# Optimization experiments

Hardware: AMD Instinct MI355X
Metric: run time of the kernel (lower is better)

## Reference

```python
import jax, jax.numpy as jnp
import numpy as np

B, S, D_IN, D_OUT, R = 8, 2048, 2048, 2048, 16

def setup_inputs() -> dict:
    key = jax.random.key(0)
    k = jax.random.split(key, 5)
    scale_w = 1.0 / np.sqrt(D_IN)
    return {
        "x": jax.random.normal(k[0], (B, S, D_IN), dtype=jnp.float32),
        "A_params": jax.random.normal(k[1], (B, D_OUT, R), dtype=jnp.float32) * 0.02,
        "B_params": jax.random.normal(k[2], (B, R, D_IN), dtype=jnp.float32) * 0.02,
        "W": jax.random.normal(k[3], (D_OUT, D_IN), dtype=jnp.float32) * scale_w,
        "b": jax.random.normal(k[4], (D_OUT,), dtype=jnp.float32) * scale_w,
    }

def reference(x, A_params, B_params, W, b):
    # base: x @ W^T + b  -> [B, S, out]
    base_out = jnp.einsum("bsi,oi->bso", x, W) + b
    # intermediate = x @ B^T -> [B, S, r]
    intermediate = jnp.einsum("bsi,bri->bsr", x, B_params)
    # adaptation = intermediate @ A^T -> [B, S, out]
    adaptation = jnp.einsum("bsr,bor->bso", intermediate, A_params)
    return base_out + adaptation
```

## Files before the change

kernel.cpp:

```cpp
#include <hip/hip_runtime.h>
#include <cstdint>
#include <cstddef>

typedef __attribute__((ext_vector_type(4))) float  floatx4;
typedef __attribute__((ext_vector_type(8))) __bf16 bf16x8;
typedef __attribute__((ext_vector_type(8))) unsigned short u16x8;

#define M_TOT 16384
#define N_TOT 2048
#define K_TOT 2048
#define NBATCH 8
#define RLORA 16

__device__ __forceinline__ unsigned short f32_to_bf16(float f) {
  unsigned u = __float_as_uint(f);
  u += 0x7fffu + ((u >> 16) & 1u);
  return (unsigned short)(u >> 16);
}

#define GLOAD_LDS16(gp, lp)                                                        \
  __builtin_amdgcn_global_load_lds((__attribute__((address_space(1))) void*)(void*)(gp), \
                                   (__attribute__((address_space(3))) void*)(void*)(lp), \
                                   16, 0, 0)

__global__ void k_convert(const float* __restrict__ in, unsigned short* __restrict__ out, int n8) {
  int i = blockIdx.x * blockDim.x + threadIdx.x;
  if (i >= n8) return;
  const float4* p = (const float4*)in + (size_t)i * 2;
  float4 v0 = p[0], v1 = p[1];
  u16x8 o;
  o[0] = f32_to_bf16(v0.x); o[1] = f32_to_bf16(v0.y);
  o[2] = f32_to_bf16(v0.z); o[3] = f32_to_bf16(v0.w);
  o[4] = f32_to_bf16(v1.x); o[5] = f32_to_bf16(v1.y);
  o[6] = f32_to_bf16(v1.z); o[7] = f32_to_bf16(v1.w);
  *(u16x8*)(out + (size_t)i * 8) = o;
}

__global__ void k_convert_a(const float* __restrict__ A, unsigned short* __restrict__ abf) {
  int row = blockIdx.x * blockDim.x + threadIdx.x;
  if (row >= NBATCH * N_TOT) return;
  const float4* p = (const float4*)(A + (size_t)row * RLORA);
  float4 v0 = p[0], v1 = p[1], v2 = p[2], v3 = p[3];
  u16x8 lo, hi2, z = {0,0,0,0,0,0,0,0};
  lo[0] = f32_to_bf16(v0.x); lo[1] = f32_to_bf16(v0.y);
  lo[2] = f32_to_bf16(v0.z); lo[3] = f32_to_bf16(v0.w);
  lo[4] = f32_to_bf16(v1.x); lo[5] = f32_to_bf16(v1.y);
  lo[6] = f32_to_bf16(v1.z); lo[7] = f32_to_bf16(v1.w);
  hi2[0] = f32_to_bf16(v2.x); hi2[1] = f32_to_bf16(v2.y);
  hi2[2] = f32_to_bf16(v2.z); hi2[3] = f32_to_bf16(v2.w);
  hi2[4] = f32_to_bf16(v3.x); hi2[5] = f32_to_bf16(v3.y);
  hi2[6] = f32_to_bf16(v3.z); hi2[7] = f32_to_bf16(v3.w);
  u16x8* dst = (u16x8*)(abf + (size_t)row * 32);
  dst[0] = lo; dst[1] = hi2; dst[2] = z; dst[3] = z;
}

__global__ __launch_bounds__(256) void k_inter(const unsigned short* __restrict__ xbf,
                                               const unsigned short* __restrict__ bpbf,
                                               unsigned short* __restrict__ interbf) {
  const int tid  = threadIdx.x;
  const int lane = tid & 63;
  const int wv   = tid >> 6;
  const int l15  = lane & 15;
  const int hi   = lane >> 4;
  const int m0   = blockIdx.x * 64;
  const int bb   = m0 >> 11;

  floatx4 zero = {0.f, 0.f, 0.f, 0.f};
  floatx4 acc[4] = {zero, zero, zero, zero};

  const unsigned short* bpb = bpbf + (size_t)bb * (RLORA * K_TOT);
  const int kb0 = wv * 512;
  for (int kb = kb0; kb < kb0 + 512; kb += 32) {
    bf16x8 bfr = *(const bf16x8*)(bpb + (size_t)l15 * K_TOT + kb + hi * 8);
    #pragma unroll
    for (int mi = 0; mi < 4; ++mi) {
      bf16x8 afr = *(const bf16x8*)(xbf + (size_t)(m0 + mi * 16 + l15) * K_TOT + kb + hi * 8);
      acc[mi] = __builtin_amdgcn_mfma_f32_16x16x32_bf16(afr, bfr, acc[mi], 0, 0, 0);
    }
  }

  __shared__ floatx4 red[4][4][64];
  #pragma unroll
  for (int mi = 0; mi < 4; ++mi) red[wv][mi][lane] = acc[mi];
  __syncthreads();
  if (wv == 0) {
    #pragma unroll
    for (int mi = 0; mi < 4; ++mi) {
      floatx4 s = red[0][mi][lane] + red[1][mi][lane] + red[2][mi][lane] + red[3][mi][lane];
      #pragma unroll
      for (int j = 0; j < 4; ++j) {
        int m = m0 + mi * 16 + hi * 4 + j;
        interbf[(size_t)m * 32 + l15] = f32_to_bf16(s[j]);
        interbf[(size_t)m * 32 + 16 + l15] = 0;
      }
    }
  }
}

__global__ __launch_bounds__(256) void k_gemm(const unsigned short* __restrict__ xbf,
                                              const unsigned short* __restrict__ wbf,
                                              const unsigned short* __restrict__ interbf,
                                              const unsigned short* __restrict__ abf,
                                              const float* __restrict__ bias,
                                              float* __restrict__ out) {
  __shared__ unsigned short As[128 * 64];
  __shared__ unsigned short Bs[128 * 64];
  const int tid  = threadIdx.x;
  const int lane = tid & 63;
  const int wv   = tid >> 6;
  const int wm   = wv >> 1, wn = wv & 1;
  const int l15  = lane & 15;
  const int hi   = lane >> 4;

  int bid  = blockIdx.x;
  int swzb = ((bid & 7) << 8) | (bid >> 3);
  const int mt = swzb >> 4;
  const int nt = swzb & 15;
  const int mrow0 = mt << 7;
  const int ncol0 = nt << 7;
  const int bb = mrow0 >> 11;

  const int m0 = mrow0 + wm * 64;
  const int n0 = ncol0 + wn * 64;

  floatx4 acc[4][4];
  {
    bf16x8 la[4], lb[4];
    #pragma unroll
    for (int mi = 0; mi < 4; ++mi)
      la[mi] = *(const bf16x8*)(interbf + (size_t)(m0 + mi * 16 + l15) * 32 + hi * 8);
    #pragma unroll
    for (int ni = 0; ni < 4; ++ni)
      lb[ni] = *(const bf16x8*)(abf + ((size_t)bb * N_TOT + n0 + ni * 16 + l15) * 32 + hi * 8);
    floatx4 z = {0.f, 0.f, 0.f, 0.f};
    #pragma unroll
    for (int mi = 0; mi < 4; ++mi)
      #pragma unroll
      for (int ni = 0; ni < 4; ++ni)
        acc[mi][ni] = __builtin_amdgcn_mfma_f32_16x16x32_bf16(la[mi], lb[ni], z, 0, 0, 0);
  }

  const unsigned short* Ag = xbf + (size_t)mrow0 * K_TOT;
  const unsigned short* Bg = wbf + (size_t)ncol0 * K_TOT;
  const unsigned short* pA[4];
  const unsigned short* pB[4];
  int ldsOff[4];
  #pragma unroll
  for (int i = 0; i < 4; ++i) {
    int c   = i * 256 + wv * 64 + lane;
    int row = c >> 3;
    int k8  = (c & 7) ^ (row & 7);
    pA[i] = Ag + (size_t)row * K_TOT + k8 * 8;
    pB[i] = Bg + (size_t)row * K_TOT + k8 * 8;
    ldsOff[i] = (i * 256 + wv * 64) * 16;
  }

  for (int kt = 0; kt < K_TOT; kt += 64) {
    #pragma unroll
    for (int i = 0; i < 4; ++i) GLOAD_LDS16(pA[i] + kt, (char*)As + ldsOff[i]);
    #pragma unroll
    for (int i = 0; i < 4; ++i) GLOAD_LDS16(pB[i] + kt, (char*)Bs + ldsOff[i]);
    asm volatile("s_waitcnt vmcnt(0)" ::: "memory");
    __syncthreads();

    #pragma unroll
    for (int ks = 0; ks < 2; ++ks) {
      bf16x8 af[4], bfv[4];
      #pragma unroll
      for (int mi = 0; mi < 4; ++mi) {
        int row = wm * 64 + mi * 16 + l15;
        int k8  = (ks * 4 + hi) ^ (row & 7);
        af[mi] = *(const bf16x8*)((const char*)As + row * 128 + k8 * 16);
      }
      #pragma unroll
      for (int ni = 0; ni < 4; ++ni) {
        int row = wn * 64 + ni * 16 + l15;
        int k8  = (ks * 4 + hi) ^ (row & 7);
        bfv[ni] = *(const bf16x8*)((const char*)Bs + row * 128 + k8 * 16);
      }
      #pragma unroll
      for (int mi = 0; mi < 4; ++mi)
        #pragma unroll
        for (int ni = 0; ni < 4; ++ni)
          acc[mi][ni] = __builtin_amdgcn_mfma_f32_16x16x32_bf16(af[mi], bfv[ni], acc[mi][ni], 0, 0, 0);
    }
    __syncthreads();
  }

  #pragma unroll
  for (int ni = 0; ni < 4; ++ni) {
    int col = n0 + ni * 16 + l15;
    float bv = bias[col];
    #pragma unroll
    for (int mi = 0; mi < 4; ++mi) {
      int r0 = m0 + mi * 16 + hi * 4;
      #pragma unroll
      for (int j = 0; j < 4; ++j)
        out[(size_t)(r0 + j) * N_TOT + col] = acc[mi][ni][j] + bv;
    }
  }
}

extern "C" void kernel_launch(void* const* d_in, const int* in_sizes, int n_in,
                              void* d_out, int out_size, void* d_ws, size_t ws_size,
                              hipStream_t stream) {
  const float* x    = (const float*)d_in[0];
  const float* Ap   = (const float*)d_in[1];
  const float* Bp   = (const float*)d_in[2];
  const float* W    = (const float*)d_in[3];
  const float* bias = (const float*)d_in[4];
  float* out = (float*)d_out;

  char* ws = (char*)d_ws;
  unsigned short* xbf     = (unsigned short*)(ws);
  unsigned short* wbf     = (unsigned short*)(ws + 67108864);
  unsigned short* abf     = (unsigned short*)(ws + 67108864 + 8388608);
  unsigned short* bpbf    = (unsigned short*)(ws + 67108864 + 8388608 + 1048576);
  unsigned short* interbf = (unsigned short*)(ws + 67108864 + 8388608 + 1048576 + 524288);

  k_convert<<<dim3(16384), dim3(256), 0, stream>>>(x,  xbf,  4194304);
  k_convert<<<dim3(2048),  dim3(256), 0, stream>>>(W,  wbf,   524288);
  k_convert<<<dim3(128),   dim3(256), 0, stream>>>(Bp, bpbf,   32768);
  k_convert_a<<<dim3(64),  dim3(256), 0, stream>>>(Ap, abf);

  k_inter<<<dim3(256), dim3(256), 0, stream>>>(xbf, bpbf, interbf);

  k_gemm<<<dim3(2048), dim3(256), 0, stream>>>(xbf, wbf, interbf, abf, bias, out);
}
```

Measured before the change: 200.5 us.

## Rewrite main GEMM as 256x256 tile, 8-wave, double-buffered pipelined kernel

Tiles grow from 128x128 with 4 waves to 256x256 with 8 waves. Each wave now computes a 128x64 sub-tile. Global-to-LDS loads are double-buffered and staged in quarter-tile pieces interleaved with four MFMA phases, using barriers, partial vmcnt waits and s_setprio to overlap memory with compute. This replaces the old load-wait-compute loop that exposed latency every k-step, and raises arithmetic intensity per LDS byte. The cost is more registers (32 accumulators per wave), 64KB of LDS per block, and intricate hand-scheduled synchronization that may hide hazards.

```diff
diff --git a/kernel.cpp b/kernel.cpp
--- a/kernel.cpp
+++ b/kernel.cpp
@@ -11,6 +11,7 @@
 #define K_TOT 2048
 #define NBATCH 8
 #define RLORA 16
+#define NT 32
 
 __device__ __forceinline__ unsigned short f32_to_bf16(float f) {
   unsigned u = __float_as_uint(f);
@@ -22,6 +23,8 @@
   __builtin_amdgcn_global_load_lds((__attribute__((address_space(1))) void*)(void*)(gp), \
                                    (__attribute__((address_space(3))) void*)(void*)(lp), \
                                    16, 0, 0)
+
+template<int V> struct IC { static constexpr int value = V; };
 
 __global__ void k_convert(const float* __restrict__ in, unsigned short* __restrict__ out, int n8) {
   int i = blockIdx.x * blockDim.x + threadIdx.x;
@@ -97,106 +100,169 @@
   }
 }
 
-__global__ __launch_bounds__(256) void k_gemm(const unsigned short* __restrict__ xbf,
-                                              const unsigned short* __restrict__ wbf,
-                                              const unsigned short* __restrict__ interbf,
-                                              const unsigned short* __restrict__ abf,
-                                              const float* __restrict__ bias,
-                                              float* __restrict__ out) {
-  __shared__ unsigned short As[128 * 64];
-  __shared__ unsigned short Bs[128 * 64];
+#define STAGE_A(bufi, h, tt) do {                                                      \
+  GLOAD_LDS16(Ag + (h)*262144 + (tt)*64 + gOff0, AsB + ((bufi)*2+(h))*16384 + ldsB0);  \
+  GLOAD_LDS16(Ag + (h)*262144 + (tt)*64 + gOff1, AsB + ((bufi)*2+(h))*16384 + ldsB1);  \
+} while(0)
+#define STAGE_B(bufi, h, tt) do {                                                      \
+  GLOAD_LDS16(Bg + (h)*262144 + (tt)*64 + gOff0, BsB + ((bufi)*2+(h))*16384 + ldsB0);  \
+  GLOAD_LDS16(Bg + (h)*262144 + (tt)*64 + gOff1, BsB + ((bufi)*2+(h))*16384 + ldsB1);  \
+} while(0)
+#define LDA(bufi, qm, mi, ks) (*(const bf16x8*)(AsB + ((bufi)*2 + wm)*16384 + \
+  ((qm)*64 + (mi)*16 + l15)*128 + ((((ks)*4 + hi) ^ swz) * 16)))
+#define LDB(bufi, ni, ks)     (*(const bf16x8*)(BsB + ((bufi)*2 + (wn>>1))*16384 + \
+  (((wn&1)*64 + (ni)*16 + l15)*128 + ((((ks)*4 + hi) ^ swz) * 16))))
+
+__global__ __launch_bounds__(512, 2) void k_gemm(const unsigned short* __restrict__ xbf,
+                                                 const unsigned short* __restrict__ wbf,
+                                                 const unsigned short* __restrict__ interbf,
+                                                 const unsigned short* __restrict__ abf,
+                                                 const float* __restrict__ bias,
+                                                 float* __restrict__ out) {
+  __shared__ unsigned short As[2][2][8192];
+  __shared__ unsigned short Bs[2][2][8192];
   const int tid  = threadIdx.x;
   const int lane = tid & 63;
-  const int wv   = tid >> 6;
-  const int wm   = wv >> 1, wn = wv & 1;
+  const int wid  = tid >> 6;
+  const int wm   = wid >> 2;
+  const int wn   = wid & 3;
   const int l15  = lane & 15;
   const int hi   = lane >> 4;
+  const int swz  = l15 & 7;
 
   int bid  = blockIdx.x;
-  int swzb = ((bid & 7) << 8) | (bid >> 3);
-  const int mt = swzb >> 4;
-  const int nt = swzb & 15;
-  const int mrow0 = mt << 7;
-  const int ncol0 = nt << 7;
+  int swzb = ((bid & 7) << 6) | (bid >> 3);
+  const int mt = swzb >> 3;
+  const int nt = swzb & 7;
+  const int mrow0 = mt << 8;
+  const int ncol0 = nt << 8;
   const int bb = mrow0 >> 11;
 
-  const int m0 = mrow0 + wm * 64;
+  const int m0 = mrow0 + wm * 128;
   const int n0 = ncol0 + wn * 64;
 
-  floatx4 acc[4][4];
+  const unsigned short* Ag = xbf + (size_t)mrow0 * K_TOT;
+  const unsigned short* Bg = wbf + (size_t)ncol0 * K_TOT;
+  char* AsB = (char*)As;
+  char* BsB = (char*)Bs;
+
+  const int r0    = tid >> 3;
+  const int k80   = (tid & 7) ^ (r0 & 7);
+  const int gOff0 = r0 * K_TOT + k80 * 8;
+  const int gOff1 = gOff0 + 64 * K_TOT;
+  const int ldsB0 = wid * 1024;
+  const int ldsB1 = 8192 + wid * 1024;
+
+  floatx4 acc[8][4];
   {
-    bf16x8 la[4], lb[4];
-    #pragma unroll
-    for (int mi = 0; mi < 4; ++mi)
+    bf16x8 la[8], lb[4];
+    #pragma unroll
+    for (int mi = 0; mi < 8; ++mi)
       la[mi] = *(const bf16x8*)(interbf + (size_t)(m0 + mi * 16 + l15) * 32 + hi * 8);
     #pragma unroll
     for (int ni = 0; ni < 4; ++ni)
       lb[ni] = *(const bf16x8*)(abf + ((size_t)bb * N_TOT + n0 + ni * 16 + l15) * 32 + hi * 8);
+
+    STAGE_B(0, 0, 0); STAGE_B(0, 1, 0); STAGE_A(0, 0, 0); STAGE_A(0, 1, 0);
+    STAGE_B(1, 0, 1); STAGE_B(1, 1, 1); STAGE_A(1, 0, 1);
+
     floatx4 z = {0.f, 0.f, 0.f, 0.f};
     #pragma unroll
-    for (int mi = 0; mi < 4; ++mi)
+    for (int mi = 0; mi < 8; ++mi)
       #pragma unroll
       for (int ni = 0; ni < 4; ++ni)
         acc[mi][ni] = __builtin_amdgcn_mfma_f32_16x16x32_bf16(la[mi], lb[ni], z, 0, 0, 0);
   }
-
-  const unsigned short* Ag = xbf + (size_t)mrow0 * K_TOT;
-  const unsigned short* Bg = wbf + (size_t)ncol0 * K_TOT;
-  const unsigned short* pA[4];
-  const unsigned short* pB[4];
-  int ldsOff[4];
-  #pragma unroll
-  for (int i = 0; i < 4; ++i) {
-    int c   = i * 256 + wv * 64 + lane;
-    int row = c >> 3;
-    int k8  = (c & 7) ^ (row & 7);
-    pA[i] = Ag + (size_t)row * K_TOT + k8 * 8;
-    pB[i] = Bg + (size_t)row * K_TOT + k8 * 8;
-    ldsOff[i] = (i * 256 + wv * 64) * 16;
-  }
-
-  for (int kt = 0; kt < K_TOT; kt += 64) {
-    #pragma unroll
-    for (int i = 0; i < 4; ++i) GLOAD_LDS16(pA[i] + kt, (char*)As + ldsOff[i]);
-    #pragma unroll
-    for (int i = 0; i < 4; ++i) GLOAD_LDS16(pB[i] + kt, (char*)Bs + ldsOff[i]);
-    asm volatile("s_waitcnt vmcnt(0)" ::: "memory");
-    __syncthreads();
-
-    #pragma unroll
-    for (int ks = 0; ks < 2; ++ks) {
-      bf16x8 af[4], bfv[4];
-      #pragma unroll
-      for (int mi = 0; mi < 4; ++mi) {
-        int row = wm * 64 + mi * 16 + l15;
-        int k8  = (ks * 4 + hi) ^ (row & 7);
-        af[mi] = *(const bf16x8*)((const char*)As + row * 128 + k8 * 16);
-      }
-      #pragma unroll
-      for (int ni = 0; ni < 4; ++ni) {
-        int row = wn * 64 + ni * 16 + l15;
-        int k8  = (ks * 4 + hi) ^ (row & 7);
-        bfv[ni] = *(const bf16x8*)((const char*)Bs + row * 128 + k8 * 16);
-      }
-      #pragma unroll
-      for (int mi = 0; mi < 4; ++mi)
-        #pragma unroll
-        for (int ni = 0; ni < 4; ++ni)
-          acc[mi][ni] = __builtin_amdgcn_mfma_f32_16x16x32_bf16(af[mi], bfv[ni], acc[mi][ni], 0, 0, 0);
-    }
-    __syncthreads();
-  }
+  asm volatile("s_waitcnt vmcnt(6)" ::: "memory");
+  __builtin_amdgcn_s_barrier();
+
+  auto tile = [&](int t, auto s1_, auto s2_, auto vm_) {
+    constexpr int S1 = decltype(s1_)::value;
+    constexpr int S2 = decltype(s2_)::value;
+    constexpr int VM = decltype(vm_)::value;
+    const int buf = t & 1;
+    bf16x8 af[4][2], bfr[4][2];
+
+    #pragma unroll
+    for (int mi = 0; mi < 4; ++mi) { af[mi][0] = LDA(buf, 0, mi, 0); af[mi][1] = LDA(buf, 0, mi, 1); }
+    #pragma unroll
+    for (int ni = 0; ni < 2; ++ni) { bfr[ni][0] = LDB(buf, ni, 0); bfr[ni][1] = LDB(buf, ni, 1); }
+    if constexpr (S1) STAGE_A(buf ^ 1, 1, t + 1);
+    __builtin_amdgcn_s_barrier();
+    asm volatile("s_waitcnt lgkmcnt(0)" ::: "memory");
+    __builtin_amdgcn_s_setprio(1);
+    #pragma unroll
+    for (int mi = 0; mi < 4; ++mi)
+      #pragma unroll
+      for (int ni = 0; ni < 2; ++ni) {
+        acc[mi][ni] = __builtin_amdgcn_mfma_f32_16x16x32_bf16(af[mi][0], bfr[ni][0], acc[mi][ni], 0, 0, 0);
+        acc[mi][ni] = __builtin_amdgcn_mfma_f32_16x16x32_bf16(af[mi][1], bfr[ni][1], acc[mi][ni], 0, 0, 0);
+      }
+    __builtin_amdgcn_s_setprio(0);
+    __builtin_amdgcn_s_barrier();
+
+    #pragma unroll
+    for (int ni = 0; ni < 2; ++ni) { bfr[2+ni][0] = LDB(buf, 2+ni, 0); bfr[2+ni][1] = LDB(buf, 2+ni, 1); }
+    __builtin_amdgcn_s_barrier();
+    asm volatile("s_waitcnt lgkmcnt(0)" ::: "memory");
+    __builtin_amdgcn_s_setprio(1);
+    #pragma unroll
+    for (int mi = 0; mi < 4; ++mi)
+      #pragma unroll
+      for (int ni = 0; ni < 2; ++ni) {
+        acc[mi][2+ni] = __builtin_amdgcn_mfma_f32_16x16x32_bf16(af[mi][0], bfr[2+ni][0], acc[mi][2+ni], 0, 0, 0);
+        acc[mi][2+ni] = __builtin_amdgcn_mfma_f32_16x16x32_bf16(af[mi][1], bfr[2+ni][1], acc[mi][2+ni], 0, 0, 0);
+      }
+    __builtin_amdgcn_s_setprio(0);
+    __builtin_amdgcn_s_barrier();
+
+    #pragma unroll
+    for (int mi = 0; mi < 4; ++mi) { af[mi][0] = LDA(buf, 1, mi, 0); af[mi][1] = LDA(buf, 1, mi, 1); }
+    if constexpr (S2) { STAGE_B(buf, 0, t + 2); STAGE_B(buf, 1, t + 2); }
+    __builtin_amdgcn_s_barrier();
+    asm volatile("s_waitcnt lgkmcnt(0)" ::: "memory");
+    __builtin_amdgcn_s_setprio(1);
+    #pragma unroll
+    for (int mi = 0; mi < 4; ++mi)
+      #pragma unroll
+      for (int ni = 0; ni < 2; ++ni) {
+        acc[4+mi][ni] = __builtin_amdgcn_mfma_f32_16x16x32_bf16(af[mi][0], bfr[ni][0], acc[4+mi][ni], 0, 0, 0);
+        acc[4+mi][ni] = __builtin_amdgcn_mfma_f32_16x16x32_bf16(af[mi][1], bfr[ni][1], acc[4+mi][ni], 0, 0, 0);
+      }
+    __builtin_amdgcn_s_setprio(0);
+    __builtin_amdgcn_s_barrier();
+
+    if constexpr (S2) STAGE_A(buf, 0, t + 2);
+    __builtin_amdgcn_s_barrier();
+    asm volatile("s_waitcnt lgkmcnt(0)" ::: "memory");
+    __builtin_amdgcn_s_setprio(1);
+    #pragma unroll
+    for (int mi = 0; mi < 4; ++mi)
+      #pragma unroll
+      for (int ni = 0; ni < 2; ++ni) {
+        acc[4+mi][2+ni] = __builtin_amdgcn_mfma_f32_16x16x32_bf16(af[mi][0], bfr[2+ni][0], acc[4+mi][2+ni], 0, 0, 0);
+        acc[4+mi][2+ni] = __builtin_amdgcn_mfma_f32_16x16x32_bf16(af[mi][1], bfr[2+ni][1], acc[4+mi][2+ni], 0, 0, 0);
+      }
+    __builtin_amdgcn_s_setprio(0);
+    if constexpr (VM == 6)      asm volatile("s_waitcnt vmcnt(6)" ::: "memory");
+    else if constexpr (VM == 0) asm volatile("s_waitcnt vmcnt(0)" ::: "memory");
+    __builtin_amdgcn_s_barrier();
+  };
+
+  for (int t = 0; t < NT - 2; ++t) tile(t, IC<1>{}, IC<1>{}, IC<6>{});
+  tile(NT - 2, IC<1>{}, IC<0>{}, IC<0>{});
+  tile(NT - 1, IC<0>{}, IC<0>{}, IC<-1>{});
 
   #pragma unroll
   for (int ni = 0; ni < 4; ++ni) {
     int col = n0 + ni * 16 + l15;
     float bv = bias[col];
     #pragma unroll
-    for (int mi = 0; mi < 4; ++mi) {
-      int r0 = m0 + mi * 16 + hi * 4;
+    for (int mi = 0; mi < 8; ++mi) {
+      int r = m0 + mi * 16 + hi * 4;
       #pragma unroll
       for (int j = 0; j < 4; ++j)
-        out[(size_t)(r0 + j) * N_TOT + col] = acc[mi][ni][j] + bv;
+        out[(size_t)(r + j) * N_TOT + col] = acc[mi][ni][j] + bv;
     }
   }
 }
@@ -225,5 +291,5 @@
 
   k_inter<<<dim3(256), dim3(256), 0, stream>>>(xbf, bpbf, interbf);
 
-  k_gemm<<<dim3(2048), dim3(256), 0, stream>>>(xbf, wbf, interbf, abf, bias, out);
-}
+  k_gemm<<<dim3(512), dim3(512), 0, stream>>>(xbf, wbf, interbf, abf, bias, out);
+}
```

Measured after the change: 210.0 us. +4.7%, slower.

## Fuse LoRA intermediate projection into main GEMM and merge conversion kernels

Applied to the files above, without the earlier changes.

Removes the separate k_inter kernel. The x@B^T LoRA projection is now computed inside the main GEMM k-loop, reusing the x tiles already staged in LDS, and the B_params slice is streamed into a small extra LDS buffer. The intermediate is written to LDS and applied with A after the loop instead of as an initial MFMA. The W/B/A conversions are also merged into one launch, and the x conversion loops over 8 elements per thread. This saves a full extra read of bf16 x and two launches, at the cost of redundant intermediate MFMAs across the 16 N-tiles and extra LDS traffic per iteration.

```diff
diff --git a/kernel.cpp b/kernel.cpp
--- a/kernel.cpp
+++ b/kernel.cpp
@@ -18,99 +18,68 @@
   return (unsigned short)(u >> 16);
 }
 
+__device__ __forceinline__ u16x8 cvt8(const float4& a, const float4& b) {
+  u16x8 o;
+  o[0] = f32_to_bf16(a.x); o[1] = f32_to_bf16(a.y);
+  o[2] = f32_to_bf16(a.z); o[3] = f32_to_bf16(a.w);
+  o[4] = f32_to_bf16(b.x); o[5] = f32_to_bf16(b.y);
+  o[6] = f32_to_bf16(b.z); o[7] = f32_to_bf16(b.w);
+  return o;
+}
+
 #define GLOAD_LDS16(gp, lp)                                                        \
   __builtin_amdgcn_global_load_lds((__attribute__((address_space(1))) void*)(void*)(gp), \
                                    (__attribute__((address_space(3))) void*)(void*)(lp), \
                                    16, 0, 0)
 
-__global__ void k_convert(const float* __restrict__ in, unsigned short* __restrict__ out, int n8) {
-  int i = blockIdx.x * blockDim.x + threadIdx.x;
-  if (i >= n8) return;
-  const float4* p = (const float4*)in + (size_t)i * 2;
-  float4 v0 = p[0], v1 = p[1];
-  u16x8 o;
-  o[0] = f32_to_bf16(v0.x); o[1] = f32_to_bf16(v0.y);
-  o[2] = f32_to_bf16(v0.z); o[3] = f32_to_bf16(v0.w);
-  o[4] = f32_to_bf16(v1.x); o[5] = f32_to_bf16(v1.y);
-  o[6] = f32_to_bf16(v1.z); o[7] = f32_to_bf16(v1.w);
-  *(u16x8*)(out + (size_t)i * 8) = o;
-}
-
-__global__ void k_convert_a(const float* __restrict__ A, unsigned short* __restrict__ abf) {
-  int row = blockIdx.x * blockDim.x + threadIdx.x;
-  if (row >= NBATCH * N_TOT) return;
-  const float4* p = (const float4*)(A + (size_t)row * RLORA);
-  float4 v0 = p[0], v1 = p[1], v2 = p[2], v3 = p[3];
-  u16x8 lo, hi2, z = {0,0,0,0,0,0,0,0};
-  lo[0] = f32_to_bf16(v0.x); lo[1] = f32_to_bf16(v0.y);
-  lo[2] = f32_to_bf16(v0.z); lo[3] = f32_to_bf16(v0.w);
-  lo[4] = f32_to_bf16(v1.x); lo[5] = f32_to_bf16(v1.y);
-  lo[6] = f32_to_bf16(v1.z); lo[7] = f32_to_bf16(v1.w);
-  hi2[0] = f32_to_bf16(v2.x); hi2[1] = f32_to_bf16(v2.y);
-  hi2[2] = f32_to_bf16(v2.z); hi2[3] = f32_to_bf16(v2.w);
-  hi2[4] = f32_to_bf16(v3.x); hi2[5] = f32_to_bf16(v3.y);
-  hi2[6] = f32_to_bf16(v3.z); hi2[7] = f32_to_bf16(v3.w);
-  u16x8* dst = (u16x8*)(abf + (size_t)row * 32);
-  dst[0] = lo; dst[1] = hi2; dst[2] = z; dst[3] = z;
-}
-
-__global__ __launch_bounds__(256) void k_inter(const unsigned short* __restrict__ xbf,
-                                               const unsigned short* __restrict__ bpbf,
-                                               unsigned short* __restrict__ interbf) {
-  const int tid  = threadIdx.x;
-  const int lane = tid & 63;
-  const int wv   = tid >> 6;
-  const int l15  = lane & 15;
-  const int hi   = lane >> 4;
-  const int m0   = blockIdx.x * 64;
-  const int bb   = m0 >> 11;
-
-  floatx4 zero = {0.f, 0.f, 0.f, 0.f};
-  floatx4 acc[4] = {zero, zero, zero, zero};
-
-  const unsigned short* bpb = bpbf + (size_t)bb * (RLORA * K_TOT);
-  const int kb0 = wv * 512;
-  for (int kb = kb0; kb < kb0 + 512; kb += 32) {
-    bf16x8 bfr = *(const bf16x8*)(bpb + (size_t)l15 * K_TOT + kb + hi * 8);
-    #pragma unroll
-    for (int mi = 0; mi < 4; ++mi) {
-      bf16x8 afr = *(const bf16x8*)(xbf + (size_t)(m0 + mi * 16 + l15) * K_TOT + kb + hi * 8);
-      acc[mi] = __builtin_amdgcn_mfma_f32_16x16x32_bf16(afr, bfr, acc[mi], 0, 0, 0);
-    }
-  }
-
-  __shared__ floatx4 red[4][4][64];
-  #pragma unroll
-  for (int mi = 0; mi < 4; ++mi) red[wv][mi][lane] = acc[mi];
-  __syncthreads();
-  if (wv == 0) {
-    #pragma unroll
-    for (int mi = 0; mi < 4; ++mi) {
-      floatx4 s = red[0][mi][lane] + red[1][mi][lane] + red[2][mi][lane] + red[3][mi][lane];
-      #pragma unroll
-      for (int j = 0; j < 4; ++j) {
-        int m = m0 + mi * 16 + hi * 4 + j;
-        interbf[(size_t)m * 32 + l15] = f32_to_bf16(s[j]);
-        interbf[(size_t)m * 32 + 16 + l15] = 0;
-      }
-    }
+__global__ void k_convert_x(const float* __restrict__ in, unsigned short* __restrict__ out) {
+  int i0 = blockIdx.x * blockDim.x + threadIdx.x;
+  #pragma unroll
+  for (int it = 0; it < 8; ++it) {
+    size_t i = (size_t)i0 + (size_t)it * 524288;
+    const float4* p = (const float4*)in + i * 2;
+    *(u16x8*)(out + i * 8) = cvt8(p[0], p[1]);
+  }
+}
+
+__global__ void k_convert_small(const float* __restrict__ W, const float* __restrict__ Bp,
+                                const float* __restrict__ Ap,
+                                unsigned short* __restrict__ wbf, unsigned short* __restrict__ bpbf,
+                                unsigned short* __restrict__ abf) {
+  int b = blockIdx.x;
+  if (b < 2048) {
+    int i = b * 256 + threadIdx.x;
+    const float4* p = (const float4*)W + (size_t)i * 2;
+    *(u16x8*)(wbf + (size_t)i * 8) = cvt8(p[0], p[1]);
+  } else if (b < 2176) {
+    int i = (b - 2048) * 256 + threadIdx.x;
+    const float4* p = (const float4*)Bp + (size_t)i * 2;
+    *(u16x8*)(bpbf + (size_t)i * 8) = cvt8(p[0], p[1]);
+  } else {
+    int row = (b - 2176) * 256 + threadIdx.x;
+    const float4* p = (const float4*)(Ap + (size_t)row * RLORA);
+    u16x8 lo = cvt8(p[0], p[1]), hi2 = cvt8(p[2], p[3]), z = {0,0,0,0,0,0,0,0};
+    u16x8* dst = (u16x8*)(abf + (size_t)row * 32);
+    dst[0] = lo; dst[1] = hi2; dst[2] = z; dst[3] = z;
   }
 }
 
 __global__ __launch_bounds__(256) void k_gemm(const unsigned short* __restrict__ xbf,
                                               const unsigned short* __restrict__ wbf,
-                                              const unsigned short* __restrict__ interbf,
+                                              const unsigned short* __restrict__ bpbf,
                                               const unsigned short* __restrict__ abf,
                                               const float* __restrict__ bias,
                                               float* __restrict__ out) {
   __shared__ unsigned short As[128 * 64];
   __shared__ unsigned short Bs[128 * 64];
+  __shared__ unsigned short BpL[16 * 64];
   const int tid  = threadIdx.x;
   const int lane = tid & 63;
   const int wv   = tid >> 6;
   const int wm   = wv >> 1, wn = wv & 1;
   const int l15  = lane & 15;
   const int hi   = lane >> 4;
+  const int swz  = l15 & 7;
 
   int bid  = blockIdx.x;
   int swzb = ((bid & 7) << 8) | (bid >> 3);
@@ -123,25 +92,9 @@
   const int m0 = mrow0 + wm * 64;
   const int n0 = ncol0 + wn * 64;
 
-  floatx4 acc[4][4];
-  {
-    bf16x8 la[4], lb[4];
-    #pragma unroll
-    for (int mi = 0; mi < 4; ++mi)
-      la[mi] = *(const bf16x8*)(interbf + (size_t)(m0 + mi * 16 + l15) * 32 + hi * 8);
-    #pragma unroll
-    for (int ni = 0; ni < 4; ++ni)
-      lb[ni] = *(const bf16x8*)(abf + ((size_t)bb * N_TOT + n0 + ni * 16 + l15) * 32 + hi * 8);
-    floatx4 z = {0.f, 0.f, 0.f, 0.f};
-    #pragma unroll
-    for (int mi = 0; mi < 4; ++mi)
-      #pragma unroll
-      for (int ni = 0; ni < 4; ++ni)
-        acc[mi][ni] = __builtin_amdgcn_mfma_f32_16x16x32_bf16(la[mi], lb[ni], z, 0, 0, 0);
-  }
-
-  const unsigned short* Ag = xbf + (size_t)mrow0 * K_TOT;
-  const unsigned short* Bg = wbf + (size_t)ncol0 * K_TOT;
+  const unsigned short* Ag  = xbf  + (size_t)mrow0 * K_TOT;
+  const unsigned short* Bg  = wbf  + (size_t)ncol0 * K_TOT;
+  const unsigned short* Bpg = bpbf + (size_t)bb * (RLORA * K_TOT);
   const unsigned short* pA[4];
   const unsigned short* pB[4];
   int ldsOff[4];
@@ -154,12 +107,23 @@
     pB[i] = Bg + (size_t)row * K_TOT + k8 * 8;
     ldsOff[i] = (i * 256 + wv * 64) * 16;
   }
+  const int bpr   = tid >> 3;
+  const int bpOff = bpr * K_TOT + ((tid & 7) ^ (bpr & 7)) * 8;
+
+  floatx4 zero = {0.f, 0.f, 0.f, 0.f};
+  floatx4 acc[4][4];
+  #pragma unroll
+  for (int mi = 0; mi < 4; ++mi)
+    #pragma unroll
+    for (int ni = 0; ni < 4; ++ni) acc[mi][ni] = zero;
+  floatx4 accI[2] = {zero, zero};
 
   for (int kt = 0; kt < K_TOT; kt += 64) {
     #pragma unroll
     for (int i = 0; i < 4; ++i) GLOAD_LDS16(pA[i] + kt, (char*)As + ldsOff[i]);
     #pragma unroll
     for (int i = 0; i < 4; ++i) GLOAD_LDS16(pB[i] + kt, (char*)Bs + ldsOff[i]);
+    if (wv < 2) GLOAD_LDS16(Bpg + kt + bpOff, (char*)BpL + wv * 1024);
     asm volatile("s_waitcnt vmcnt(0)" ::: "memory");
     __syncthreads();
 
@@ -178,14 +142,49 @@
         int k8  = (ks * 4 + hi) ^ (row & 7);
         bfv[ni] = *(const bf16x8*)((const char*)Bs + row * 128 + k8 * 16);
       }
+      bf16x8 bpf = *(const bf16x8*)((const char*)BpL + l15 * 128 + (((ks * 4 + hi) ^ swz) * 16));
       #pragma unroll
       for (int mi = 0; mi < 4; ++mi)
         #pragma unroll
         for (int ni = 0; ni < 4; ++ni)
           acc[mi][ni] = __builtin_amdgcn_mfma_f32_16x16x32_bf16(af[mi], bfv[ni], acc[mi][ni], 0, 0, 0);
+      if (wn == 0) {
+        accI[0] = __builtin_amdgcn_mfma_f32_16x16x32_bf16(af[0], bpf, accI[0], 0, 0, 0);
+        accI[1] = __builtin_amdgcn_mfma_f32_16x16x32_bf16(af[1], bpf, accI[1], 0, 0, 0);
+      } else {
+        accI[0] = __builtin_amdgcn_mfma_f32_16x16x32_bf16(af[2], bpf, accI[0], 0, 0, 0);
+        accI[1] = __builtin_amdgcn_mfma_f32_16x16x32_bf16(af[3], bpf, accI[1], 0, 0, 0);
+      }
     }
     __syncthreads();
   }
+
+  bf16x8 lb[4];
+  #pragma unroll
+  for (int ni = 0; ni < 4; ++ni)
+    lb[ni] = *(const bf16x8*)(abf + ((size_t)bb * N_TOT + n0 + ni * 16 + l15) * 32 + hi * 8);
+
+  unsigned short* interL = As;
+  #pragma unroll
+  for (int p = 0; p < 2; ++p) {
+    #pragma unroll
+    for (int j = 0; j < 4; ++j) {
+      int row = wm * 64 + (2 * wn + p) * 16 + hi * 4 + j;
+      interL[row * 32 + l15]      = f32_to_bf16(accI[p][j]);
+      interL[row * 32 + 16 + l15] = 0;
+    }
+  }
+  __syncthreads();
+
+  bf16x8 la[4];
+  #pragma unroll
+  for (int mi = 0; mi < 4; ++mi)
+    la[mi] = *(const bf16x8*)(interL + (wm * 64 + mi * 16 + l15) * 32 + hi * 8);
+  #pragma unroll
+  for (int mi = 0; mi < 4; ++mi)
+    #pragma unroll
+    for (int ni = 0; ni < 4; ++ni)
+      acc[mi][ni] = __builtin_amdgcn_mfma_f32_16x16x32_bf16(la[mi], lb[ni], acc[mi][ni], 0, 0, 0);
 
   #pragma unroll
   for (int ni = 0; ni < 4; ++ni) {
@@ -212,18 +211,12 @@
   float* out = (float*)d_out;
 
   char* ws = (char*)d_ws;
-  unsigned short* xbf     = (unsigned short*)(ws);
-  unsigned short* wbf     = (unsigned short*)(ws + 67108864);
-  unsigned short* abf     = (unsigned short*)(ws + 67108864 + 8388608);
-  unsigned short* bpbf    = (unsigned short*)(ws + 67108864 + 8388608 + 1048576);
-  unsigned short* interbf = (unsigned short*)(ws + 67108864 + 8388608 + 1048576 + 524288);
-
-  k_convert<<<dim3(16384), dim3(256), 0, stream>>>(x,  xbf,  4194304);
-  k_convert<<<dim3(2048),  dim3(256), 0, stream>>>(W,  wbf,   524288);
-  k_convert<<<dim3(128),   dim3(256), 0, stream>>>(Bp, bpbf,   32768);
-  k_convert_a<<<dim3(64),  dim3(256), 0, stream>>>(Ap, abf);
-
-  k_inter<<<dim3(256), dim3(256), 0, stream>>>(xbf, bpbf, interbf);
-
-  k_gemm<<<dim3(2048), dim3(256), 0, stream>>>(xbf, wbf, interbf, abf, bias, out);
-}
+  unsigned short* xbf  = (unsigned short*)(ws);
+  unsigned short* wbf  = (unsigned short*)(ws + 67108864);
+  unsigned short* abf  = (unsigned short*)(ws + 67108864 + 8388608);
+  unsigned short* bpbf = (unsigned short*)(ws + 67108864 + 8388608 + 1048576);
+
+  k_convert_small<<<dim3(2240), dim3(256), 0, stream>>>(W, Bp, Ap, wbf, bpbf, abf);
+  k_convert_x<<<dim3(2048), dim3(256), 0, stream>>>(x, xbf);
+  k_gemm<<<dim3(2048), dim3(256), 0, stream>>>(xbf, wbf, bpbf, abf, bias, out);
+}
```

Result: slower. 223.7 us (+11.6%).
